# Optimization experiments

Measured on AMD Instinct MI355X. Metric: run time of the kernel, lower is better.

Reference implementation:

```python
import jax, jax.numpy as jnp
import numpy as np
from jax import lax

# Dims: B queries, N nodes, E edges (inverse edges already included), D hidden,
# R2 = 2*num_relation, T tail candidates, M text-embedded nodes, L layers.
B, N, E, D, R2, T, M, L = 4, 50000, 1600000, 64, 1000, 32, 10000, 3
NODE_RATIO, DEG_RATIO = 0.1, 1.0
K = int(NODE_RATIO * N)              # nodes kept per layer (variadic_topks on node scores)
ESEL = int(DEG_RATIO * K * E / N)    # edges kept per layer


def setup_inputs():
    key = jax.random.key(0)
    ks = jax.random.split(key, 16)
    f32 = jnp.float32
    return {
        "h_index": jax.random.randint(ks[0], (B,), 0, N),
        "r_index": jax.random.randint(ks[1], (B,), 0, R2),
        "t_index": jax.random.randint(ks[2], (B, T), 0, N),
        "all_index": jax.random.randint(ks[3], (M,), 0, N),
        "edge_src": jax.random.randint(ks[4], (E,), 0, N),
        "edge_dst": jax.random.randint(ks[5], (E,), 0, N),
        "edge_type": jax.random.randint(ks[6], (E,), 0, R2),
        "hidden_states": jax.random.normal(ks[7], (B, D), f32),
        "score_text_embs": jax.random.normal(ks[8], (M, D), f32),
        "rel_table": 0.02 * jax.random.normal(ks[9], (R2, D), f32),
        "linear_w": jax.random.normal(ks[10], (2 * D, D), f32) / np.sqrt(2 * D),
        "linear_b": jnp.zeros((D,), f32),
        "mlp_w1": jax.random.normal(ks[11], (D, 2 * D), f32) / np.sqrt(D),
        "mlp_b1": jnp.zeros((2 * D,), f32),
        "mlp_w2": jax.random.normal(ks[12], (2 * D, 1), f32) / np.sqrt(2 * D),
        "mlp_b2": jnp.zeros((1,), f32),
        "relw": 0.1 * jax.random.normal(ks[13], (L, R2, D), f32),
        "pna_w": jax.random.normal(ks[14], (L, 12 * D, D), f32) / np.sqrt(12 * D),
        "pna_b": jnp.zeros((L, D), f32),
    }


def _forward(h_index, r_index, t_index, all_index, edge_src, edge_dst, edge_type,
             hidden_states, score_text_embs, rel_table, linear_w, linear_b,
             mlp_w1, mlp_b1, mlp_w2, mlp_b2, relw, pna_w, pna_b):
    def score_fn(hidden, rel):  # hidden [n, D], rel [D] -> [n]
        rel_b = jnp.broadcast_to(rel, hidden.shape)
        heur = jnp.concatenate([hidden, rel_b], -1) @ linear_w + linear_b
        x = hidden * heur
        h1 = jax.nn.relu(x @ mlp_w1 + mlp_b1)
        return jnp.squeeze(h1 @ mlp_w2 + mlp_b2, -1)

    # pna_degree_mean = mean(log(degree_out + 1)) over the base graph
    deg_out_full = jax.ops.segment_sum(jnp.ones((E,), jnp.float32), edge_src, num_segments=N)
    dmean = jnp.mean(jnp.log(deg_out_full + 1.0))

    rel_embeds = rel_table[r_index]  # [B, D]

    def per_batch(rel, h_idx, head_emb, t_idx):
        # init_input_embeds: text embeddings at all_index, head embedding at h_idx
        hidden = (jnp.zeros((N, D), jnp.float32)
                  .at[all_index].set(score_text_embs)
                  .at[h_idx].set(head_emb))
        base = score_fn(jnp.zeros((1, D), jnp.float32), rel)[0]
        score = jnp.full((N,), base, jnp.float32).at[h_idx].set(score_fn(head_emb[None], rel)[0])

        for l in range(L):
            # ---- select_edges: top-K nodes by score, then top-ESEL outgoing edges by dst score
            _, nidx = lax.top_k(score, K)
            sel = jnp.zeros((N,), bool).at[nidx].set(True)
            escore = jnp.where(sel[edge_src], score[edge_dst], -jnp.inf)
            ev, eidx = lax.top_k(escore, ESEL)
            valid = jnp.isfinite(ev)
            s, d, et = edge_src[eidx], edge_dst[eidx], edge_type[eidx]

            # ---- gated message passing on the selected subgraph (PNA aggregation)
            gate = jax.nn.sigmoid(score)
            msg = (gate[s, None] * hidden[s]) * relw[l][et]        # [ESEL, D]
            msg0 = jnp.where(valid[:, None], msg, 0.0)
            deg = jax.ops.segment_sum(valid.astype(jnp.float32), d, num_segments=N)
            sm = jax.ops.segment_sum(msg0, d, num_segments=N)
            sq = jax.ops.segment_sum(msg0 * msg0, d, num_segments=N)
            mx = jax.ops.segment_max(jnp.where(valid[:, None], msg, -jnp.inf), d, num_segments=N)
            mn = jax.ops.segment_min(jnp.where(valid[:, None], msg, jnp.inf), d, num_segments=N)
            has = (deg > 0.0)[:, None]
            degc = jnp.maximum(deg, 1.0)[:, None]
            mean = sm / degc
            std = jnp.where(has, jnp.sqrt(jax.nn.relu(sq / degc - mean * mean) + 1e-6), 0.0)
            mx = jnp.where(has, mx, 0.0)
            mn = jnp.where(has, mn, 0.0)
            logd = jnp.log(deg + 1.0)[:, None]
            amp = logd / dmean
            att = jnp.where(has, dmean / jnp.maximum(logd, 1e-6), 0.0)
            one = jnp.ones_like(amp)
            # 4 aggregators x 3 degree scalers -> [N, 12D]
            feats = jnp.concatenate([a * sc for a in (mean, mx, mn, std) for sc in (one, amp, att)], -1)
            out = feats @ pna_w[l] + pna_b[l]

            # scatter back: only nodes with subgraph out-degree > 0 are updated
            hidden = jnp.where(has, hidden + out, hidden)
            score = jnp.where(deg > 0.0, score_fn(hidden, rel), score)
        return score[t_idx]

    return jax.vmap(per_batch)(rel_embeds, h_index, hidden_states, t_index)  # [B, T]


def reference(h_index, r_index, t_index, all_index, edge_src, edge_dst, edge_type,
              hidden_states, score_text_embs, rel_table, linear_w, linear_b,
              mlp_w1, mlp_b1, mlp_w2, mlp_b2, relw, pna_w, pna_b):
    return _forward(h_index, r_index, t_index, all_index, edge_src, edge_dst, edge_type,
                    hidden_states, score_text_embs, rel_table, linear_w, linear_b,
                    mlp_w1, mlp_b1, mlp_w2, mlp_b2, relw, pna_w, pna_b)
```

## Files before the change

kernel.cpp:

```cpp
#include <hip/hip_runtime.h>
#include <cstdint>
#include <cstddef>


#define NN   50000
#define NEG  1600000
#define NR2  1000
#define NTC  32
#define NMI  10000
#define KSEL 5000u
#define ESEL 160000u
#define KEY_NEG_INF 0x007FFFFFu

#define OFF_ST    0
#define OFF_RELB  64
#define OFF_BC    128
#define OFF_BC2   2176
#define OFF_HISTA 4224
#define OFF_HISTB 69760
#define OFF_SCORE 135296
#define OFF_NSEL  185296
#define OFF_DCNT  235296
#define OFF_ROWS  285296
#define OFF_CURS  335296
#define OFF_ACT   385296
#define OFF_HID   435296
#define OFF_SRCH  3635296
#define OFF_ELIST 3955296
#define OFF_CSR   4115296
#define OFF_BALG  (OFF_CSR + 50032)
#define SBLK      4275296

#define RL(x,k) __int_as_float(__builtin_amdgcn_readlane(__float_as_int(x),(k)))
#define BBASE unsigned* B = WB + (size_t)blockIdx.y * (size_t)sb

__device__ inline unsigned fkey(float f){
  unsigned u = __float_as_uint(f);
  if ((u << 1) == 0u) u = 0u;
  return (u & 0x80000000u) ? ~u : (u | 0x80000000u);
}

__device__ inline float waveSumF(float v){
  #pragma unroll
  for (int d = 1; d < 64; d <<= 1) v += __shfl_xor(v, d);
  return v;
}

__device__ inline void ldsHashAdd(unsigned* hkey, unsigned* hval, unsigned bin, unsigned cnt){
  unsigned h = (bin * 2654435761u) >> 23;
  while (true){
    unsigned prev = atomicCAS(hkey + h, 0xFFFFFFFFu, bin);
    if (prev == 0xFFFFFFFFu || prev == bin){ atomicAdd(hval + h, cnt); return; }
    h = (h + 1u) & 511u;
  }
}


__global__ void k_lastm(const int* __restrict__ all_index, int* __restrict__ lastm){
  int i = blockIdx.x * 256 + threadIdx.x;
  if (i < NMI) atomicMax(lastm + all_index[i], i);
}

__global__ void k_degfull(const int* __restrict__ esrc, unsigned* __restrict__ degf){
  int i = blockIdx.x * 256 + threadIdx.x;
  if (i < NEG) atomicAdd(degf + esrc[i], 1u);
}

__global__ void k_dsum(const unsigned* __restrict__ degf, float* __restrict__ gstF){
  int i = blockIdx.x * 256 + threadIdx.x;
  float v = (i < NN) ? logf((float)degf[i] + 1.f) : 0.f;
  v = waveSumF(v);
  if ((threadIdx.x & 63) == 0) atomicAdd(gstF + 4, v);
}

__global__ void k_finalize(float* __restrict__ gstF, const float* __restrict__ b1,
                           const float* __restrict__ w2, const float* __restrict__ b2){
  gstF[5] = gstF[4] / (float)NN;
  float s = 0.f;
  for (int m = 0; m < 128; m++) s += fmaxf(b1[m], 0.f) * w2[m];
  gstF[6] = s + b2[0];
}


__global__ void k_relb(unsigned* WB, long sb, int b0,
                       const int* __restrict__ r_index, const float* __restrict__ hs,
                       const float* __restrict__ rel_table, const float* __restrict__ lw,
                       const float* __restrict__ lb, const float* __restrict__ w1,
                       const float* __restrict__ b1, const float* __restrict__ w2,
                       const float* __restrict__ b2){
  BBASE;
  float* relb = (float*)(B + OFF_RELB);
  float* stF  = (float*)(B + OFF_ST);
  int b = b0 + blockIdx.y;
  int j = threadIdx.x;
  int r = r_index[b];
  float acc = lb[j];
  for (int k = 0; k < 64; k++) acc = fmaf(rel_table[(size_t)r*64 + k], lw[(64 + k)*64 + j], acc);
  relb[j] = acc;
  float heur = acc;
  for (int k = 0; k < 64; k++) heur = fmaf(hs[b*64 + k], lw[k*64 + j], heur);
  float x = hs[b*64 + j] * heur;
  float o = 0.f;
  for (int half = 0; half < 2; half++){
    float a = b1[half*64 + j];
    for (int k = 0; k < 64; k++) a = fmaf(__shfl(x, k), w1[k*128 + half*64 + j], a);
    o = fmaf(fmaxf(a, 0.f), w2[half*64 + j], o);
  }
  o = waveSumF(o);
  if (j == 0) stF[7] = o + b2[0];
}

__global__ void k_inithidden(unsigned* WB, long sb, int b0,
                             const int* __restrict__ lastm, const float* __restrict__ ste,
                             const float* __restrict__ hs, const int* __restrict__ h_index){
  BBASE;
  float4* hidden = (float4*)(B + OFF_HID);
  const float4* ste4 = (const float4*)ste;
  const float4* hs4  = (const float4*)hs;
  int b = b0 + blockIdx.y;
  int idx = blockIdx.x * 256 + threadIdx.x;
  int n = idx >> 4, j = idx & 15;
  int h = h_index[b];
  float4 v = make_float4(0.f, 0.f, 0.f, 0.f);
  int lm = lastm[n];
  if (lm >= 0) v = ste4[(size_t)lm*16 + j];
  if (n == h)  v = hs4[b*16 + j];
  hidden[idx] = v;
}

__global__ void k_initscore(unsigned* WB, long sb, int b0,
                            const int* __restrict__ h_index, const float* __restrict__ gstF){
  BBASE;
  float* score = (float*)(B + OFF_SCORE);
  unsigned* st = B + OFF_ST;
  float* stF = (float*)st;
  int b = b0 + blockIdx.y;
  int i = blockIdx.x * 256 + threadIdx.x;
  if (i < NN) score[i] = (i == h_index[b]) ? stF[7] : gstF[6];
  if (i == 0){ st[0] = 0u; st[1] = KSEL; }
}


__global__ __launch_bounds__(256) void k_hist(unsigned* WB, long sb, int pass){
  BBASE;
  const unsigned* st = B + OFF_ST;
  const float* score = (const float*)(B + OFF_SCORE);
  unsigned* hist = B + ((pass == 1) ? OFF_HISTA : OFF_HISTB);
  __shared__ unsigned hkey[512];
  __shared__ unsigned hval[512];
  for (int t = threadIdx.x; t < 512; t += 256){ hkey[t] = 0xFFFFFFFFu; hval[t] = 0u; }
  __syncthreads();
  int i = blockIdx.x * 256 + threadIdx.x;
  unsigned bin = 0xFFFFFFFFu;
  if (i < NN){
    unsigned k = fkey(score[i]);
    if (pass == 1) bin = k >> 16;
    else if ((k >> 16) == (st[0] >> 16)) bin = k & 0xFFFFu;
  }
  bool active = (bin != 0xFFFFFFFFu);
  int lane = threadIdx.x & 63;
  #pragma unroll
  for (int r = 0; r < 2; r++){
    unsigned long long mask = __ballot((int)active);
    if (mask != 0ull){
      int leader = __ffsll(mask) - 1;
      unsigned lbin = (unsigned)__shfl((int)bin, leader);
      bool same = active && (bin == lbin);
      unsigned long long smask = __ballot((int)same);
      if (lane == leader) ldsHashAdd(hkey, hval, lbin, (unsigned)__popcll(smask));
      if (same) active = false;
    }
  }
  if (active) ldsHashAdd(hkey, hval, bin, 1u);
  __syncthreads();
  for (int t = threadIdx.x; t < 512; t += 256){
    unsigned vv = hval[t];
    if (vv) atomicAdd(hist + hkey[t], vv);
  }
}

__global__ void k_indegW(unsigned* WB, long sb,
                         const int* __restrict__ esrc, const int* __restrict__ edst){
  BBASE;
  unsigned* st = B + OFF_ST;
  const unsigned* nsel = B + OFF_NSEL;
  unsigned* indeg = B + OFF_CURS;
  int i = blockIdx.x * 256 + threadIdx.x;
  if (i < NEG && nsel[esrc[i]]) atomicAdd(indeg + edst[i], 1u);
  if (i == 0){ st[0] = 0u; st[1] = ESEL; st[2] = 0u; st[3] = 0u; st[4] = 0u; st[5] = 0u; }
}

__global__ __launch_bounds__(256) void k_histW(unsigned* WB, long sb, int pass){
  BBASE;
  const unsigned* st = B + OFF_ST;
  const unsigned* indeg = B + OFF_CURS;
  const float* score = (const float*)(B + OFF_SCORE);
  unsigned* hist = B + ((pass == 1) ? OFF_HISTA : OFF_HISTB);
  __shared__ unsigned hkey[512];
  __shared__ unsigned hval[512];
  for (int t = threadIdx.x; t < 512; t += 256){ hkey[t] = 0xFFFFFFFFu; hval[t] = 0u; }
  __syncthreads();
  int i = blockIdx.x * 256 + threadIdx.x;
  unsigned w = (i < NN) ? indeg[i] : 0u;
  if (w){
    unsigned k = fkey(score[i]);
    unsigned bin = 0xFFFFFFFFu;
    if (pass == 1) bin = k >> 16;
    else if ((k >> 16) == (st[0] >> 16)) bin = k & 0xFFFFu;
    if (bin != 0xFFFFFFFFu) ldsHashAdd(hkey, hval, bin, w);
  }
  __syncthreads();
  for (int t = threadIdx.x; t < 512; t += 256){
    unsigned vv = hval[t];
    if (vv) atomicAdd(hist + hkey[t], vv);
  }
}

__global__ __launch_bounds__(1024) void k_pick16(unsigned* WB, long sb, int pass){
  BBASE;
  unsigned* st = B + OFF_ST;
  const unsigned* hist = B + ((pass == 1) ? OFF_HISTA : OFF_HISTB);
  __shared__ unsigned csum[1024];
  __shared__ unsigned sc[1024];
  int t = threadIdx.x;
  unsigned R = st[1];
  unsigned s = 0;
  {
    const unsigned* hp = hist + (unsigned)t * 64u;
    for (int b = 0; b < 64; b++) s += hp[b];
  }
  csum[t] = s; sc[t] = s; __syncthreads();
  for (int d = 1; d < 1024; d <<= 1){
    unsigned v = (t >= d) ? sc[t - d] : 0u;
    __syncthreads();
    sc[t] += v;
    __syncthreads();
  }
  unsigned total = sc[1023];
  unsigned above = total - sc[t];
  unsigned cs = csum[t];
  if (above < R && above + cs >= R){
    unsigned cum = above;
    for (int b = 63; b >= 0; b--){
      unsigned c = hist[(unsigned)(t*64 + b)];
      if (cum + c >= R){
        unsigned bstar = (unsigned)(t*64 + b);
        if (pass == 1) st[0] = bstar << 16; else st[0] = st[0] | bstar;
        st[1] = R - cum;
        break;
      }
      cum += c;
    }
  }
  if (t == 0 && total < R){
    if (pass == 1) st[0] = KEY_NEG_INF & 0xFFFF0000u;
    else           st[0] = st[0] | 0xFFFFu;
    st[1] = R - total;
  }
}

__global__ __launch_bounds__(1024) void k_countEq(unsigned* WB, long sb, int mode, int n,
                                                  const int* __restrict__ esrc,
                                                  const int* __restrict__ edst){
  BBASE;
  unsigned* hz = B + OFF_HISTA;
  for (unsigned j = blockIdx.x * 1024u + threadIdx.x; j < 131072u; j += gridDim.x * 1024u)
    hz[j] = 0u;
  unsigned* dcnt = B + OFF_DCNT;
  const unsigned* st = B + OFF_ST;
  const unsigned* nsel = B + OFF_NSEL;
  const float* score = (const float*)(B + OFF_SCORE);
  unsigned* bcE = B + OFF_BC;
  unsigned* bcG = B + OFF_BC2;
  unsigned* balE = B + OFF_CSR;
  unsigned* balG = B + OFF_BALG;
  int i = blockIdx.x * 1024 + threadIdx.x;
  if (i < NN) dcnt[i] = 0u;
  unsigned v = st[0];
  unsigned k = 0u;
  if (i < n){
    if (mode) k = nsel[esrc[i]] ? fkey(score[edst[i]]) : KEY_NEG_INF;
    else      k = fkey(score[i]);
  }
  bool eq = (i < n) && (k == v);
  bool gt = (i < n) && (k > v);
  unsigned long long ebal = __ballot((int)eq);
  unsigned long long gbal = __ballot((int)gt);
  __shared__ unsigned wshE[16];
  __shared__ unsigned wshG[16];
  int wid = threadIdx.x >> 6, lane = threadIdx.x & 63;
  if (mode && lane == 0){
    int gw = blockIdx.x * 16 + wid;
    balE[2*gw]     = (unsigned)ebal;
    balE[2*gw + 1] = (unsigned)(ebal >> 32);
    balG[2*gw]     = (unsigned)gbal;
    balG[2*gw + 1] = (unsigned)(gbal >> 32);
  }
  if (lane == 0){ wshE[wid] = (unsigned)__popcll(ebal); wshG[wid] = (unsigned)__popcll(gbal); }
  __syncthreads();
  if (threadIdx.x == 0){
    unsigned te = 0, tg = 0;
    for (int w = 0; w < 16; w++){ te += wshE[w]; tg += wshG[w]; }
    bcE[blockIdx.x] = te; bcG[blockIdx.x] = tg;
  }
}

__global__ __launch_bounds__(1024) void k_scanBlocks(unsigned* WB, long sb, int nbk){
  BBASE;
  unsigned* blockcnt = B + OFF_BC;
  __shared__ unsigned sc[2048];
  int t = threadIdx.x;
  unsigned a  = (t < nbk) ? blockcnt[t] : 0u;
  unsigned b2 = (1024 + t < nbk) ? blockcnt[1024 + t] : 0u;
  sc[t] = a; sc[1024 + t] = b2; __syncthreads();
  for (int d = 1; d < 2048; d <<= 1){
    unsigned v1 = (t >= d) ? sc[t - d] : 0u;
    unsigned v2 = (1024 + t >= d) ? sc[1024 + t - d] : 0u;
    __syncthreads();
    sc[t] += v1; sc[1024 + t] += v2;
    __syncthreads();
  }
  if (t < nbk) blockcnt[t] = sc[t] - a;
  if (1024 + t < nbk) blockcnt[1024 + t] = sc[1024 + t] - b2;
}

__global__ __launch_bounds__(1024) void k_scanBlocks2(unsigned* WB, long sb, int nbk){
  BBASE;
  unsigned* st = B + OFF_ST;
  unsigned* bcE = B + OFF_BC;
  unsigned* bcG = B + OFF_BC2;
  __shared__ unsigned se[2048];
  __shared__ unsigned sg[2048];
  int t = threadIdx.x;
  unsigned e0 = (t < nbk) ? bcE[t] : 0u;
  unsigned e1 = (1024 + t < nbk) ? bcE[1024 + t] : 0u;
  unsigned g0 = (t < nbk) ? bcG[t] : 0u;
  unsigned g1 = (1024 + t < nbk) ? bcG[1024 + t] : 0u;
  se[t] = e0; se[1024 + t] = e1; sg[t] = g0; sg[1024 + t] = g1;
  __syncthreads();
  for (int d = 1; d < 2048; d <<= 1){
    unsigned a1 = (t >= d) ? se[t - d] : 0u;
    unsigned a2 = (1024 + t >= d) ? se[1024 + t - d] : 0u;
    unsigned c1 = (t >= d) ? sg[t - d] : 0u;
    unsigned c2 = (1024 + t >= d) ? sg[1024 + t - d] : 0u;
    __syncthreads();
    se[t] += a1; se[1024 + t] += a2; sg[t] += c1; sg[1024 + t] += c2;
    __syncthreads();
  }
  if (t < nbk) bcE[t] = se[t] - e0;
  if (1024 + t < nbk) bcE[1024 + t] = se[1024 + t] - e1;
  if (t < nbk) bcG[t] = sg[t] - g0;
  if (1024 + t < nbk) bcG[1024 + t] = sg[1024 + t] - g1;
  if (t == 0){
    unsigned gtTot = sg[2047];
    st[4] = gtTot;
    st[2] = gtTot + ((st[0] > KEY_NEG_INF) ? st[1] : 0u);
  }
}

__global__ __launch_bounds__(1024) void k_selNodes(unsigned* WB, long sb){
  BBASE;
  const unsigned* st = B + OFF_ST;
  const unsigned* blockcnt = B + OFF_BC;
  const float* score = (const float*)(B + OFF_SCORE);
  unsigned* nsel = B + OFF_NSEL;
  unsigned* curs = B + OFF_CURS;
  int i = blockIdx.x * 1024 + threadIdx.x;
  if (i < NN) curs[i] = 0u;
  unsigned v = st[0], R = st[1];
  unsigned k = (i < NN) ? fkey(score[i]) : 0u;
  bool eq = (i < NN) && (k == v);
  unsigned long long bal = __ballot((int)eq);
  __shared__ unsigned wsh[16];
  int wid = threadIdx.x >> 6, lane = threadIdx.x & 63;
  if (lane == 0) wsh[wid] = (unsigned)__popcll(bal);
  __syncthreads();
  unsigned woff = 0;
  for (int w = 0; w < wid; w++) woff += wsh[w];
  unsigned lpre = (unsigned)__popcll(bal & ((1ull << lane) - 1ull));
  unsigned rank = blockcnt[blockIdx.x] + woff + lpre;
  if (i < NN) nsel[i] = (k > v || (eq && rank < R)) ? 1u : 0u;
}

__global__ __launch_bounds__(1024) void k_selEdgesCompact(unsigned* WB, long sb,
                                                          const int* __restrict__ esrc,
                                                          const int* __restrict__ edst){
  BBASE;
  const unsigned* st = B + OFF_ST;
  const unsigned* bcE = B + OFF_BC;
  const unsigned* bcG = B + OFF_BC2;
  const unsigned* balE = B + OFF_CSR;
  const unsigned* balG = B + OFF_BALG;
  unsigned* elist = B + OFF_ELIST;
  unsigned* dcnt = B + OFF_DCNT;
  int i = blockIdx.x * 1024 + threadIdx.x;
  unsigned v = st[0], R = st[1], gtTot = st[4];
  int wid = threadIdx.x >> 6, lane = threadIdx.x & 63;
  int gw = blockIdx.x * 16 + wid;
  unsigned long long ebal = ((unsigned long long)balE[2*gw + 1] << 32) | balE[2*gw];
  unsigned long long gbal = ((unsigned long long)balG[2*gw + 1] << 32) | balG[2*gw];
  bool eq = (ebal >> lane) & 1ull;
  bool gt = (gbal >> lane) & 1ull;
  __shared__ unsigned wshE[16];
  __shared__ unsigned wshG[16];
  if (lane == 0){ wshE[wid] = (unsigned)__popcll(ebal); wshG[wid] = (unsigned)__popcll(gbal); }
  __syncthreads();
  unsigned eoff = 0, goff = 0;
  for (int w = 0; w < 16 && w < wid; w++){ eoff += wshE[w]; goff += wshG[w]; }
  unsigned long long ltm = (1ull << lane) - 1ull;
  if (gt){
    elist[bcG[blockIdx.x] + goff + (unsigned)__popcll(gbal & ltm)] = (unsigned)i;
    atomicAdd(dcnt + edst[i], 1u);
  }
  if (eq){
    unsigned rank = bcE[blockIdx.x] + eoff + (unsigned)__popcll(ebal & ltm);
    if (v > KEY_NEG_INF && rank < R){
      elist[gtTot + rank] = (unsigned)i;
      atomicAdd(dcnt + edst[i], 1u);
    }
  }
}


__global__ __launch_bounds__(1024) void k_blocksumsInt(unsigned* WB, long sb){
  BBASE;
  const unsigned* dcnt = B + OFF_DCNT;
  unsigned* blockcnt = B + OFF_BC;
  int i = blockIdx.x * 1024 + threadIdx.x;
  unsigned v = (i < NN) ? dcnt[i] : 0u;
  #pragma unroll
  for (int d = 1; d < 64; d <<= 1) v += (unsigned)__shfl_xor((int)v, d);
  __shared__ unsigned wsh[16];
  int wid = threadIdx.x >> 6, lane = threadIdx.x & 63;
  if (lane == 0) wsh[wid] = v;
  __syncthreads();
  if (threadIdx.x == 0){
    unsigned tot = 0;
    for (int w = 0; w < 16; w++) tot += wsh[w];
    blockcnt[blockIdx.x] = tot;
  }
}

__global__ __launch_bounds__(1024) void k_rowSnap(unsigned* WB, long sb){
  BBASE;
  unsigned* st = B + OFF_ST;
  const unsigned* dcnt = B + OFF_DCNT;
  const unsigned* blockcnt = B + OFF_BC;
  unsigned* rowstart = B + OFF_ROWS;
  unsigned* curs = B + OFF_CURS;
  unsigned* actl = B + OFF_ACT;
  unsigned* srcmap = B + OFF_NSEL;
  const float* score = (const float*)(B + OFF_SCORE);
  const float* hidden = (const float*)(B + OFF_HID);
  float* srch = (float*)(B + OFF_SRCH);
  int i = blockIdx.x * 1024 + threadIdx.x;
  int wid = threadIdx.x >> 6, lane = threadIdx.x & 63;
  unsigned d = (i < NN) ? dcnt[i] : 0u;
  unsigned v = d;
  #pragma unroll
  for (int dl = 1; dl < 64; dl <<= 1){
    unsigned t2 = (unsigned)__shfl_up((int)v, dl);
    if (lane >= dl) v += t2;
  }
  bool act = (i < NN) && (d > 0u);
  unsigned long long abal = __ballot((int)act);
  __shared__ unsigned wsh[16];
  __shared__ unsigned awsh[16];
  __shared__ unsigned abase;
  if (lane == 63) wsh[wid] = v;
  if (lane == 0) awsh[wid] = (unsigned)__popcll(abal);
  __syncthreads();
  if (threadIdx.x == 0){
    unsigned tot = 0;
    for (int w = 0; w < 16; w++) tot += awsh[w];
    abase = atomicAdd(st + 3, tot);
  }
  unsigned woff = 0, aoff = 0;
  for (int w = 0; w < wid; w++){ woff += wsh[w]; aoff += awsh[w]; }
  __syncthreads();
  unsigned excl = blockcnt[blockIdx.x] + woff + (v - d);
  if (i < NN){ rowstart[i] = excl; curs[i] = excl; }
  if (act) actl[abase + aoff + (unsigned)__popcll(abal & ((1ull << lane) - 1ull))] = (unsigned)i;

  int base = i - lane;
  if (base >= NN) return;
  bool sel = (i < NN) && (srcmap[i] != 0u);
  unsigned long long bal = __ballot((int)sel);
  if (bal == 0ull) return;
  unsigned slotbase = 0;
  if (lane == 0) slotbase = atomicAdd(st + 5, (unsigned)__popcll(bal));
  slotbase = (unsigned)__shfl((int)slotbase, 0);
  unsigned long long m2 = bal;
  unsigned idx = 0;
  while (m2){
    int j = __ffsll(m2) - 1;
    m2 = m2 - (m2 bitand (0ull - m2));
    int node = base + j;
    unsigned slot = slotbase + idx; idx++;
    if (lane == 0) srcmap[node] = slot;
    float g = 1.f / (1.f + expf(-score[node]));
    srch[(size_t)slot*64 + lane] = g * hidden[(size_t)node*64 + lane];
  }
}

__global__ void k_scatter(unsigned* WB, long sb, const int* __restrict__ esrc,
                          const int* __restrict__ edst, const int* __restrict__ etype){
  BBASE;
  const unsigned* st = B + OFF_ST;
  const unsigned* elist = B + OFF_ELIST;
  const unsigned* srcmap = B + OFF_NSEL;
  unsigned* curs = B + OFF_CURS;
  unsigned* csr = B + OFF_CSR;
  unsigned i = blockIdx.x * 256 + threadIdx.x;
  if (i < st[2]){
    unsigned e = elist[i];
    unsigned slot = srcmap[esrc[e]];
    unsigned pk = (slot << 10) | (unsigned)etype[e];
    unsigned pos = atomicAdd(curs + edst[e], 1u);
    csr[pos] = pk;
  }
}


__global__ __launch_bounds__(256) void k_aggpna(unsigned* WB, long sb,
    const float* __restrict__ relw, const float* __restrict__ pw,
    const float* __restrict__ pb, const float* __restrict__ gstF, int l){
  BBASE;
  const unsigned* st = B + OFF_ST;
  const unsigned* actl = B + OFF_ACT;
  const unsigned* dcnt = B + OFF_DCNT;
  const unsigned* rows = B + OFF_ROWS;
  const unsigned* csr = B + OFF_CSR;
  const float* srch = (const float*)(B + OFF_SRCH);
  float* hidden = (float*)(B + OFF_HID);
  const float* relw_l = relw + (size_t)l * NR2 * 64;
  const float* pw_l = pw + (size_t)l * 768 * 64;

  __shared__ float aggL[64 * 64];

  int lane = threadIdx.x & 63;
  int w = threadIdx.x >> 6;
  unsigned nact = st[3];
  unsigned nbase = (unsigned)blockIdx.x * 64u;
  if (nbase >= nact) return;
  float dmean = gstF[5];

  unsigned slotM = nbase + (unsigned)lane;
  int nodeM = (slotM < nact) ? (int)actl[slotM] : -1;
  float dvM = (nodeM >= 0) ? (float)dcnt[nodeM] : 0.f;
  float logd = logf(dvM + 1.f);
  float ampv = logd / dmean;
  float attv = dmean / fmaxf(logd, 1e-6f);
  int jbase = __builtin_amdgcn_readfirstlane((int)(threadIdx.x >> 6)) * 16;
  float acc[16];
  #pragma unroll
  for (int jj = 0; jj < 16; jj++) acc[jj] = pb[(size_t)l*64 + jbase + jj];

  int nodeG[16]; unsigned cntG[16], rsG[16];
  #pragma unroll
  for (int i = 0; i < 16; i++){
    unsigned slot = nbase + (unsigned)(w * 16 + i);
    nodeG[i] = (slot < nact) ? (int)actl[slot] : -1;
  }
  #pragma unroll
  for (int i = 0; i < 16; i++){
    cntG[i] = (nodeG[i] >= 0) ? dcnt[nodeG[i]] : 0u;
    rsG[i]  = (nodeG[i] >= 0) ? rows[nodeG[i]] : 0u;
  }

  float mxS[16], mnS[16], sdS[16];
  #pragma unroll
  for (int g = 0; g < 4; g++){
    unsigned pkA[4], pkB[4], pkC[4], pkD[4];
    #pragma unroll
    for (int q = 0; q < 4; q++){
      int i = g*4 + q;
      unsigned cnt = cntG[i], rs = rsG[i];
      bool vld = (nodeG[i] >= 0);
      unsigned c1 = (1u < cnt) ? 1u : 0u;
      unsigned c2 = (2u < cnt) ? 2u : 0u;
      unsigned c3 = (3u < cnt) ? 3u : 0u;
      pkA[q] = vld ? csr[rs]      : 0u;
      pkB[q] = vld ? csr[rs + c1] : 0u;
      pkC[q] = vld ? csr[rs + c2] : 0u;
      pkD[q] = vld ? csr[rs + c3] : 0u;
    }
    #pragma unroll
    for (int q = 0; q < 4; q++){
      int i = g*4 + q;
      int nloc = w * 16 + i;
      float pmean = 0.f;
      mxS[i] = 0.f; mnS[i] = 0.f; sdS[i] = 0.f;
      if (nodeG[i] >= 0){
        unsigned cnt = cntG[i], rs = rsG[i];
        float sm_ = 0.f, sq_ = 0.f;
        float mx_ = -__builtin_huge_valf(), mn_ = __builtin_huge_valf();
        {
          unsigned pk0 = pkA[q], pk1 = pkB[q], pk2 = pkC[q], pk3 = pkD[q];
          float s0 = srch[(size_t)(pk0 >> 10)*64 + lane];
          float r0 = relw_l[(size_t)(pk0 & 1023u)*64 + lane];
          float s1 = srch[(size_t)(pk1 >> 10)*64 + lane];
          float r1 = relw_l[(size_t)(pk1 & 1023u)*64 + lane];
          float s2 = srch[(size_t)(pk2 >> 10)*64 + lane];
          float r2 = relw_l[(size_t)(pk2 & 1023u)*64 + lane];
          float s3 = srch[(size_t)(pk3 >> 10)*64 + lane];
          float r3 = relw_l[(size_t)(pk3 & 1023u)*64 + lane];
          float m = s0 * r0;
          sm_ += m; sq_ = fmaf(m, m, sq_); mx_ = fmaxf(mx_, m); mn_ = fminf(mn_, m);
          if (1u < cnt){
            m = s1 * r1;
            sm_ += m; sq_ = fmaf(m, m, sq_); mx_ = fmaxf(mx_, m); mn_ = fminf(mn_, m);
          }
          if (2u < cnt){
            m = s2 * r2;
            sm_ += m; sq_ = fmaf(m, m, sq_); mx_ = fmaxf(mx_, m); mn_ = fminf(mn_, m);
          }
          if (3u < cnt){
            m = s3 * r3;
            sm_ += m; sq_ = fmaf(m, m, sq_); mx_ = fmaxf(mx_, m); mn_ = fminf(mn_, m);
          }
        }
        for (unsigned ii = 4; ii < cnt; ii += 4u){
          unsigned i1 = (ii + 1u < cnt) ? ii + 1u : ii;
          unsigned i2 = (ii + 2u < cnt) ? ii + 2u : ii;
          unsigned i3 = (ii + 3u < cnt) ? ii + 3u : ii;
          unsigned pk0 = csr[rs + ii];
          unsigned pk1 = csr[rs + i1];
          unsigned pk2 = csr[rs + i2];
          unsigned pk3 = csr[rs + i3];
          float s0 = srch[(size_t)(pk0 >> 10)*64 + lane];
          float r0 = relw_l[(size_t)(pk0 & 1023u)*64 + lane];
          float s1 = srch[(size_t)(pk1 >> 10)*64 + lane];
          float r1 = relw_l[(size_t)(pk1 & 1023u)*64 + lane];
          float s2 = srch[(size_t)(pk2 >> 10)*64 + lane];
          float r2 = relw_l[(size_t)(pk2 & 1023u)*64 + lane];
          float s3 = srch[(size_t)(pk3 >> 10)*64 + lane];
          float r3 = relw_l[(size_t)(pk3 & 1023u)*64 + lane];
          float m = s0 * r0;
          sm_ += m; sq_ = fmaf(m, m, sq_); mx_ = fmaxf(mx_, m); mn_ = fminf(mn_, m);
          if (ii + 1u < cnt){
            m = s1 * r1;
            sm_ += m; sq_ = fmaf(m, m, sq_); mx_ = fmaxf(mx_, m); mn_ = fminf(mn_, m);
          }
          if (ii + 2u < cnt){
            m = s2 * r2;
            sm_ += m; sq_ = fmaf(m, m, sq_); mx_ = fmaxf(mx_, m); mn_ = fminf(mn_, m);
          }
          if (ii + 3u < cnt){
            m = s3 * r3;
            sm_ += m; sq_ = fmaf(m, m, sq_); mx_ = fmaxf(mx_, m); mn_ = fminf(mn_, m);
          }
        }
        float dv = (float)cnt;
        float degc = fmaxf(dv, 1.f);
        float me = sm_ / degc;
        pmean = me;
        mxS[i] = mx_;
        mnS[i] = mn_;
        sdS[i] = sqrtf(fmaxf(sq_ / degc - me*me, 0.f) + 1e-6f);
      }
      aggL[lane*64 + (nloc ^ lane)] = pmean;
    }
  }

  for (int p = 0; p < 4; p++){
    if (p){
      __syncthreads();
      #pragma unroll
      for (int i = 0; i < 16; i++){
        int nloc = w * 16 + i;
        float v = (p == 1) ? mxS[i] : ((p == 2) ? mnS[i] : sdS[i]);
        aggL[lane*64 + (nloc ^ lane)] = v;
      }
    }
    __syncthreads();
    for (int cc = 0; cc < 3; cc++){
      int c = p*3 + cc;
      float sc = (cc == 0) ? 1.f : ((cc == 1) ? ampv : attv);
      const float* wc = pw_l + (size_t)c*64*64 + jbase;
      #pragma unroll 4
      for (int k = 0; k < 64; k++){
        float fv = aggL[k*64 + (lane ^ k)] * sc;
        const float* wp = wc + (size_t)k*64;
        #pragma unroll
        for (int jj = 0; jj < 16; jj++)
          acc[jj] = fmaf(fv, wp[jj], acc[jj]);
      }
    }
  }
  if (nodeM >= 0){
    float* hp = hidden + (size_t)nodeM*64 + jbase;
    #pragma unroll
    for (int q = 0; q < 4; q++){
      float4 h = *(float4*)(hp + q*4);
      h.x += acc[q*4+0]; h.y += acc[q*4+1]; h.z += acc[q*4+2]; h.w += acc[q*4+3];
      *(float4*)(hp + q*4) = h;
    }
  }
}


__global__ __launch_bounds__(256) void k_scoreK(unsigned* WB, long sb,
    const float* __restrict__ lw, const float* __restrict__ w1,
    const float* __restrict__ b1, const float* __restrict__ w2,
    const float* __restrict__ b2){
  BBASE;
  unsigned* st = B + OFF_ST;
  if (blockIdx.x == 0 && threadIdx.x == 0){ st[0] = 0u; st[1] = KSEL; }
  const unsigned* actl = B + OFF_ACT;
  const float* hidden = (const float*)(B + OFF_HID);
  const float* relb = (const float*)(B + OFF_RELB);
  float* score = (float*)(B + OFF_SCORE);

  __shared__ float P0[64 * 64];
  __shared__ float P1[64 * 64];

  int lane = threadIdx.x & 63;
  int w = threadIdx.x >> 6;
  unsigned nact = st[3];
  unsigned nbase = (unsigned)blockIdx.x * 64u;
  if (nbase >= nact) return;

  int nodeG[16];
  #pragma unroll
  for (int i = 0; i < 16; i++){
    unsigned slot = nbase + (unsigned)(w * 16 + i);
    nodeG[i] = (slot < nact) ? (int)actl[slot] : -1;
  }
  #pragma unroll
  for (int i = 0; i < 16; i++){
    int nloc = w * 16 + i;
    float hv = (nodeG[i] >= 0) ? hidden[(size_t)nodeG[i]*64 + lane] : 0.f;
    P0[lane*64 + (nloc ^ lane)] = hv;
  }
  __syncthreads();

  int jb = __builtin_amdgcn_readfirstlane(w) * 16;
  float heur[16];
  #pragma unroll
  for (int i = 0; i < 16; i++) heur[i] = relb[jb + i];
  #pragma unroll 4
  for (int k = 0; k < 64; k++){
    float hk = P0[k*64 + (lane ^ k)];
    const float* lwk = lw + k*64 + jb;
    #pragma unroll
    for (int i = 0; i < 16; i++) heur[i] = fmaf(hk, lwk[i], heur[i]);
  }
  #pragma unroll
  for (int i = 0; i < 16; i++){
    int j = jb + i;
    float hj = P0[j*64 + (lane ^ j)];
    P1[j*64 + (lane ^ j)] = hj * heur[i];
  }
  __syncthreads();

  float alo[16], ahi[16];
  #pragma unroll
  for (int mm = 0; mm < 16; mm++){ alo[mm] = b1[jb + mm]; ahi[mm] = b1[64 + jb + mm]; }
  #pragma unroll 4
  for (int j = 0; j < 64; j++){
    float xj = P1[j*64 + (lane ^ j)];
    const float* w1j = w1 + j*128;
    #pragma unroll
    for (int mm = 0; mm < 16; mm++){
      alo[mm] = fmaf(xj, w1j[jb + mm], alo[mm]);
      ahi[mm] = fmaf(xj, w1j[64 + jb + mm], ahi[mm]);
    }
  }
  #pragma unroll
  for (int mm = 0; mm < 16; mm++){
    int j = jb + mm;
    float p = fmaf(fmaxf(alo[mm], 0.f), w2[j], 0.f);
    p = fmaf(fmaxf(ahi[mm], 0.f), w2[64 + j], p);
    P0[j*64 + (lane ^ j)] = p;
  }
  __syncthreads();

  float b2v = b2[0];
  for (int i = 0; i < 16; i++){
    int nloc = w * 16 + i;
    unsigned slot = nbase + (unsigned)nloc;
    float p = P0[lane*64 + (nloc ^ lane)];
    float r = waveSumF(p);
    if (lane == 0 && slot < nact) score[(int)actl[slot]] = r + b2v;
  }
}

__global__ void k_out(unsigned* WB, long sb, int b0,
                      const int* __restrict__ t_index, float* __restrict__ out){
  BBASE;
  const float* score = (const float*)(B + OFF_SCORE);
  int b = b0 + blockIdx.y;
  int t = threadIdx.x;
  if (t < NTC) out[b*NTC + t] = score[t_index[b*NTC + t]];
}


extern "C" void kernel_launch(void* const* d_in, const int* in_sizes, int n_in,
                              void* d_out, int out_size, void* d_ws, size_t ws_size,
                              hipStream_t stream){
  (void)in_sizes; (void)n_in; (void)out_size;
  const int*   h_index  = (const int*)d_in[0];
  const int*   r_index  = (const int*)d_in[1];
  const int*   t_index  = (const int*)d_in[2];
  const int*   all_idx  = (const int*)d_in[3];
  const int*   esrc     = (const int*)d_in[4];
  const int*   edst     = (const int*)d_in[5];
  const int*   etype    = (const int*)d_in[6];
  const float* hs       = (const float*)d_in[7];
  const float* ste      = (const float*)d_in[8];
  const float* rel_tab  = (const float*)d_in[9];
  const float* lw       = (const float*)d_in[10];
  const float* lb       = (const float*)d_in[11];
  const float* w1       = (const float*)d_in[12];
  const float* b1       = (const float*)d_in[13];
  const float* w2       = (const float*)d_in[14];
  const float* b2       = (const float*)d_in[15];
  const float* relw     = (const float*)d_in[16];
  const float* pna_w    = (const float*)d_in[17];
  const float* pna_b    = (const float*)d_in[18];
  float* out = (float*)d_out;

  unsigned* W = (unsigned*)d_ws;
  int*      LASTM = (int*)W;
  unsigned* DEGF  = W + 50000;
  float*    GSTF  = (float*)(W + 100000);
  unsigned* WB    = W + 100064;

  size_t needB = (size_t)(100064 + 4*(size_t)SBLK) * 4u;
  int nb; long sb; int nseq;
  if (ws_size >= needB){ nb = 4; sb = SBLK; nseq = 1; }
  else                 { nb = 1; sb = 0;    nseq = 4; }

  (void)hipMemsetAsync(W + 100000, 0, 64 * 4, stream);
  (void)hipMemsetAsync(LASTM, 0xFF, NN * 4, stream);
  (void)hipMemsetAsync(DEGF, 0, NN * 4, stream);
  for (int q = 0; q < nb; q++)
    (void)hipMemsetAsync(WB + (size_t)q*SBLK + OFF_HISTA, 0, 131072 * 4, stream);

  const int GB_E256  = (NEG + 255) / 256;
  const int GB_N256  = (NN + 255) / 256;
  const int GB_N1024 = (NN + 1023) / 1024;
  const int GB_E1024 = (NEG + 1023) / 1024;
  const int GB_H4    = (NN * 16) / 256;
  const int GB_A2    = (NN + 63) / 64;
  const int GB_ES    = (int)(ESEL / 256);

  k_lastm<<<(NMI + 255) / 256, 256, 0, stream>>>(all_idx, LASTM);
  k_degfull<<<GB_E256, 256, 0, stream>>>(esrc, DEGF);
  k_dsum<<<GB_N256, 256, 0, stream>>>(DEGF, GSTF);
  k_finalize<<<1, 1, 0, stream>>>(GSTF, b1, w2, b2);

  for (int q = 0; q < nseq; q++){
    int b0 = (nb == 4) ? 0 : q;
    k_relb<<<dim3(1, nb), 64, 0, stream>>>(WB, sb, b0, r_index, hs, rel_tab, lw, lb, w1, b1, w2, b2);
    k_inithidden<<<dim3(GB_H4, nb), 256, 0, stream>>>(WB, sb, b0, LASTM, ste, hs, h_index);
    k_initscore<<<dim3(GB_N256, nb), 256, 0, stream>>>(WB, sb, b0, h_index, GSTF);

    for (int l = 0; l < 3; l++){
      k_hist<<<dim3(GB_N256, nb), 256, 0, stream>>>(WB, sb, 1);
      k_pick16<<<dim3(1, nb), 1024, 0, stream>>>(WB, sb, 1);
      k_hist<<<dim3(GB_N256, nb), 256, 0, stream>>>(WB, sb, 0);
      k_pick16<<<dim3(1, nb), 1024, 0, stream>>>(WB, sb, 0);
      k_countEq<<<dim3(GB_N1024, nb), 1024, 0, stream>>>(WB, sb, 0, NN, esrc, edst);
      k_scanBlocks<<<dim3(1, nb), 1024, 0, stream>>>(WB, sb, GB_N1024);
      k_selNodes<<<dim3(GB_N1024, nb), 1024, 0, stream>>>(WB, sb);
      k_indegW<<<dim3(GB_E256, nb), 256, 0, stream>>>(WB, sb, esrc, edst);
      k_histW<<<dim3(GB_N256, nb), 256, 0, stream>>>(WB, sb, 1);
      k_pick16<<<dim3(1, nb), 1024, 0, stream>>>(WB, sb, 1);
      k_histW<<<dim3(GB_N256, nb), 256, 0, stream>>>(WB, sb, 0);
      k_pick16<<<dim3(1, nb), 1024, 0, stream>>>(WB, sb, 0);
      k_countEq<<<dim3(GB_E1024, nb), 1024, 0, stream>>>(WB, sb, 1, NEG, esrc, edst);
      k_scanBlocks2<<<dim3(1, nb), 1024, 0, stream>>>(WB, sb, GB_E1024);
      k_selEdgesCompact<<<dim3(GB_E1024, nb), 1024, 0, stream>>>(WB, sb, esrc, edst);
      k_blocksumsInt<<<dim3(GB_N1024, nb), 1024, 0, stream>>>(WB, sb);
      k_scanBlocks<<<dim3(1, nb), 1024, 0, stream>>>(WB, sb, GB_N1024);
      k_rowSnap<<<dim3(GB_N1024, nb), 1024, 0, stream>>>(WB, sb);
      k_scatter<<<dim3(GB_ES, nb), 256, 0, stream>>>(WB, sb, esrc, edst, etype);
      k_aggpna<<<dim3(GB_A2, nb), 256, 0, stream>>>(WB, sb, relw, pna_w, pna_b, GSTF, l);
      k_scoreK<<<dim3(GB_A2, nb), 256, 0, stream>>>(WB, sb, lw, w1, b1, w2, b2);
    }
    k_out<<<dim3(1, nb), 32, 0, stream>>>(WB, sb, b0, t_index, out);
  }
}
```

Measured before the change: 2.233 ms.

## Drop separate block-scan kernels and cache edge selection ballots from indegree pass

Removes the three single-block scan kernels per layer. Each consumer block now computes its own exclusive prefix by summing the preceding block counts directly: a serial loop for the node kernels, and a wave-shuffle reduction over up to 1563 counts for the edge compaction kernel. The indegree kernel also stores per-wave ballots of whether each edge's source is selected, so the edge counting pass reads a bit instead of gathering nsel[esrc[i]]. This cuts kernel launches and dependent gathers, but adds redundant prefix work in every block.

```diff
diff --git a/kernel.cpp b/kernel.cpp
--- a/kernel.cpp
+++ b/kernel.cpp
@@ -11,6 +11,8 @@
 #define KSEL 5000u
 #define ESEL 160000u
 #define KEY_NEG_INF 0x007FFFFFu
+#define NEBK 1563
+#define NWAVE_E (NEG/64)
 
 #define OFF_ST    0
 #define OFF_RELB  64
@@ -185,8 +187,17 @@
   unsigned* st = B + OFF_ST;
   const unsigned* nsel = B + OFF_NSEL;
   unsigned* indeg = B + OFF_CURS;
+  unsigned* sbal = B + OFF_ELIST;
   int i = blockIdx.x * 256 + threadIdx.x;
-  if (i < NEG && nsel[esrc[i]]) atomicAdd(indeg + edst[i], 1u);
+  int wid = threadIdx.x >> 6, lane = threadIdx.x & 63;
+  bool s = nsel[esrc[i]] != 0u;
+  unsigned long long bal = __ballot((int)s);
+  if (s) atomicAdd(indeg + edst[i], 1u);
+  if (lane == 0){
+    int gw = blockIdx.x * 4 + wid;
+    sbal[2*gw]     = (unsigned)bal;
+    sbal[2*gw + 1] = (unsigned)(bal >> 32);
+  }
   if (i == 0){ st[0] = 0u; st[1] = ESEL; st[2] = 0u; st[3] = 0u; st[4] = 0u; st[5] = 0u; }
 }
 
@@ -268,7 +279,6 @@
     hz[j] = 0u;
   unsigned* dcnt = B + OFF_DCNT;
   const unsigned* st = B + OFF_ST;
-  const unsigned* nsel = B + OFF_NSEL;
   const float* score = (const float*)(B + OFF_SCORE);
   unsigned* bcE = B + OFF_BC;
   unsigned* bcG = B + OFF_BC2;
@@ -277,18 +287,29 @@
   int i = blockIdx.x * 1024 + threadIdx.x;
   if (i < NN) dcnt[i] = 0u;
   unsigned v = st[0];
-  unsigned k = 0u;
-  if (i < n){
-    if (mode) k = nsel[esrc[i]] ? fkey(score[edst[i]]) : KEY_NEG_INF;
-    else      k = fkey(score[i]);
-  }
-  bool eq = (i < n) && (k == v);
-  bool gt = (i < n) && (k > v);
+  int wid = threadIdx.x >> 6, lane = threadIdx.x & 63;
+  bool eq = false, gt = false;
+  if (mode){
+    const unsigned* sbal = B + OFF_ELIST;
+    int gw = blockIdx.x * 16 + wid;
+    if (gw < NWAVE_E){
+      unsigned long long sb64 = ((unsigned long long)sbal[2*gw + 1] << 32) | sbal[2*gw];
+      bool ssel = (sb64 >> lane) & 1ull;
+      unsigned k = KEY_NEG_INF;
+      if (ssel) k = fkey(score[edst[i]]);
+      eq = (k == v);
+      gt = (k > v);
+    }
+  } else {
+    unsigned k = 0u;
+    if (i < n) k = fkey(score[i]);
+    eq = (i < n) && (k == v);
+    gt = (i < n) && (k > v);
+  }
   unsigned long long ebal = __ballot((int)eq);
   unsigned long long gbal = __ballot((int)gt);
   __shared__ unsigned wshE[16];
   __shared__ unsigned wshG[16];
-  int wid = threadIdx.x >> 6, lane = threadIdx.x & 63;
   if (mode && lane == 0){
     int gw = blockIdx.x * 16 + wid;
     balE[2*gw]     = (unsigned)ebal;
@@ -302,59 +323,6 @@
     unsigned te = 0, tg = 0;
     for (int w = 0; w < 16; w++){ te += wshE[w]; tg += wshG[w]; }
     bcE[blockIdx.x] = te; bcG[blockIdx.x] = tg;
-  }
-}
-
-__global__ __launch_bounds__(1024) void k_scanBlocks(unsigned* WB, long sb, int nbk){
-  BBASE;
-  unsigned* blockcnt = B + OFF_BC;
-  __shared__ unsigned sc[2048];
-  int t = threadIdx.x;
-  unsigned a  = (t < nbk) ? blockcnt[t] : 0u;
-  unsigned b2 = (1024 + t < nbk) ? blockcnt[1024 + t] : 0u;
-  sc[t] = a; sc[1024 + t] = b2; __syncthreads();
-  for (int d = 1; d < 2048; d <<= 1){
-    unsigned v1 = (t >= d) ? sc[t - d] : 0u;
-    unsigned v2 = (1024 + t >= d) ? sc[1024 + t - d] : 0u;
-    __syncthreads();
-    sc[t] += v1; sc[1024 + t] += v2;
-    __syncthreads();
-  }
-  if (t < nbk) blockcnt[t] = sc[t] - a;
-  if (1024 + t < nbk) blockcnt[1024 + t] = sc[1024 + t] - b2;
-}
-
-__global__ __launch_bounds__(1024) void k_scanBlocks2(unsigned* WB, long sb, int nbk){
-  BBASE;
-  unsigned* st = B + OFF_ST;
-  unsigned* bcE = B + OFF_BC;
-  unsigned* bcG = B + OFF_BC2;
-  __shared__ unsigned se[2048];
-  __shared__ unsigned sg[2048];
-  int t = threadIdx.x;
-  unsigned e0 = (t < nbk) ? bcE[t] : 0u;
-  unsigned e1 = (1024 + t < nbk) ? bcE[1024 + t] : 0u;
-  unsigned g0 = (t < nbk) ? bcG[t] : 0u;
-  unsigned g1 = (1024 + t < nbk) ? bcG[1024 + t] : 0u;
-  se[t] = e0; se[1024 + t] = e1; sg[t] = g0; sg[1024 + t] = g1;
-  __syncthreads();
-  for (int d = 1; d < 2048; d <<= 1){
-    unsigned a1 = (t >= d) ? se[t - d] : 0u;
-    unsigned a2 = (1024 + t >= d) ? se[1024 + t - d] : 0u;
-    unsigned c1 = (t >= d) ? sg[t - d] : 0u;
-    unsigned c2 = (1024 + t >= d) ? sg[1024 + t - d] : 0u;
-    __syncthreads();
-    se[t] += a1; se[1024 + t] += a2; sg[t] += c1; sg[1024 + t] += c2;
-    __syncthreads();
-  }
-  if (t < nbk) bcE[t] = se[t] - e0;
-  if (1024 + t < nbk) bcE[1024 + t] = se[1024 + t] - e1;
-  if (t < nbk) bcG[t] = sg[t] - g0;
-  if (1024 + t < nbk) bcG[1024 + t] = sg[1024 + t] - g1;
-  if (t == 0){
-    unsigned gtTot = sg[2047];
-    st[4] = gtTot;
-    st[2] = gtTot + ((st[0] > KEY_NEG_INF) ? st[1] : 0u);
   }
 }
 
@@ -375,10 +343,12 @@
   int wid = threadIdx.x >> 6, lane = threadIdx.x & 63;
   if (lane == 0) wsh[wid] = (unsigned)__popcll(bal);
   __syncthreads();
+  unsigned pre = 0;
+  for (int bn = 0; bn < blockIdx.x; bn++) pre += blockcnt[bn];
   unsigned woff = 0;
   for (int w = 0; w < wid; w++) woff += wsh[w];
   unsigned lpre = (unsigned)__popcll(bal & ((1ull << lane) - 1ull));
-  unsigned rank = blockcnt[blockIdx.x] + woff + lpre;
+  unsigned rank = pre + woff + lpre;
   if (i < NN) nsel[i] = (k > v || (eq && rank < R)) ? 1u : 0u;
 }
 
@@ -386,7 +356,7 @@
                                                           const int* __restrict__ esrc,
                                                           const int* __restrict__ edst){
   BBASE;
-  const unsigned* st = B + OFF_ST;
+  unsigned* st = B + OFF_ST;
   const unsigned* bcE = B + OFF_BC;
   const unsigned* bcG = B + OFF_BC2;
   const unsigned* balE = B + OFF_CSR;
@@ -394,26 +364,46 @@
   unsigned* elist = B + OFF_ELIST;
   unsigned* dcnt = B + OFF_DCNT;
   int i = blockIdx.x * 1024 + threadIdx.x;
-  unsigned v = st[0], R = st[1], gtTot = st[4];
+  unsigned v = st[0], R = st[1];
+  int t = threadIdx.x;
   int wid = threadIdx.x >> 6, lane = threadIdx.x & 63;
   int gw = blockIdx.x * 16 + wid;
   unsigned long long ebal = ((unsigned long long)balE[2*gw + 1] << 32) | balE[2*gw];
   unsigned long long gbal = ((unsigned long long)balG[2*gw + 1] << 32) | balG[2*gw];
   bool eq = (ebal >> lane) & 1ull;
   bool gt = (gbal >> lane) & 1ull;
-  __shared__ unsigned wshE[16];
-  __shared__ unsigned wshG[16];
-  if (lane == 0){ wshE[wid] = (unsigned)__popcll(ebal); wshG[wid] = (unsigned)__popcll(gbal); }
-  __syncthreads();
+  unsigned eP = 0, gP = 0, gT = 0;
+  if (t < blockIdx.x){ eP = bcE[t]; gP = bcG[t]; }
+  if (1024 + t < blockIdx.x){ eP += bcE[1024 + t]; gP += bcG[1024 + t]; }
+  if (t < NEBK) gT = bcG[t];
+  if (1024 + t < NEBK) gT += bcG[1024 + t];
+  #pragma unroll
+  for (int d = 1; d < 64; d <<= 1){
+    eP += (unsigned)__shfl_xor((int)eP, d);
+    gP += (unsigned)__shfl_xor((int)gP, d);
+    gT += (unsigned)__shfl_xor((int)gT, d);
+  }
+  __shared__ unsigned wE[16], wG[16], wT[16], wshE[16], wshG[16];
+  if (lane == 0){
+    wE[wid] = eP; wG[wid] = gP; wT[wid] = gT;
+    wshE[wid] = (unsigned)__popcll(ebal); wshG[wid] = (unsigned)__popcll(gbal);
+  }
+  __syncthreads();
+  unsigned eBase = 0, gBase = 0, gtTot = 0;
+  for (int w = 0; w < 16; w++){ eBase += wE[w]; gBase += wG[w]; gtTot += wT[w]; }
   unsigned eoff = 0, goff = 0;
-  for (int w = 0; w < 16 && w < wid; w++){ eoff += wshE[w]; goff += wshG[w]; }
+  for (int w = 0; w < wid; w++){ eoff += wshE[w]; goff += wshG[w]; }
+  if (blockIdx.x == 0 && threadIdx.x == 0){
+    st[4] = gtTot;
+    st[2] = gtTot + ((v > KEY_NEG_INF) ? R : 0u);
+  }
   unsigned long long ltm = (1ull << lane) - 1ull;
   if (gt){
-    elist[bcG[blockIdx.x] + goff + (unsigned)__popcll(gbal & ltm)] = (unsigned)i;
+    elist[gBase + goff + (unsigned)__popcll(gbal & ltm)] = (unsigned)i;
     atomicAdd(dcnt + edst[i], 1u);
   }
   if (eq){
-    unsigned rank = bcE[blockIdx.x] + eoff + (unsigned)__popcll(ebal & ltm);
+    unsigned rank = eBase + eoff + (unsigned)__popcll(ebal & ltm);
     if (v > KEY_NEG_INF && rank < R){
       elist[gtTot + rank] = (unsigned)i;
       atomicAdd(dcnt + edst[i], 1u);
@@ -475,10 +465,12 @@
     for (int w = 0; w < 16; w++) tot += awsh[w];
     abase = atomicAdd(st + 3, tot);
   }
+  unsigned pre = 0;
+  for (int bn = 0; bn < blockIdx.x; bn++) pre += blockcnt[bn];
   unsigned woff = 0, aoff = 0;
   for (int w = 0; w < wid; w++){ woff += wsh[w]; aoff += awsh[w]; }
   __syncthreads();
-  unsigned excl = blockcnt[blockIdx.x] + woff + (v - d);
+  unsigned excl = pre + woff + (v - d);
   if (i < NN){ rowstart[i] = excl; curs[i] = excl; }
   if (act) actl[abase + aoff + (unsigned)__popcll(abal & ((1ull << lane) - 1ull))] = (unsigned)i;
 
@@ -863,7 +855,6 @@
       k_hist<<<dim3(GB_N256, nb), 256, 0, stream>>>(WB, sb, 0);
       k_pick16<<<dim3(1, nb), 1024, 0, stream>>>(WB, sb, 0);
       k_countEq<<<dim3(GB_N1024, nb), 1024, 0, stream>>>(WB, sb, 0, NN, esrc, edst);
-      k_scanBlocks<<<dim3(1, nb), 1024, 0, stream>>>(WB, sb, GB_N1024);
       k_selNodes<<<dim3(GB_N1024, nb), 1024, 0, stream>>>(WB, sb);
       k_indegW<<<dim3(GB_E256, nb), 256, 0, stream>>>(WB, sb, esrc, edst);
       k_histW<<<dim3(GB_N256, nb), 256, 0, stream>>>(WB, sb, 1);
@@ -871,10 +862,8 @@
       k_histW<<<dim3(GB_N256, nb), 256, 0, stream>>>(WB, sb, 0);
       k_pick16<<<dim3(1, nb), 1024, 0, stream>>>(WB, sb, 0);
       k_countEq<<<dim3(GB_E1024, nb), 1024, 0, stream>>>(WB, sb, 1, NEG, esrc, edst);
-      k_scanBlocks2<<<dim3(1, nb), 1024, 0, stream>>>(WB, sb, GB_E1024);
       k_selEdgesCompact<<<dim3(GB_E1024, nb), 1024, 0, stream>>>(WB, sb, esrc, edst);
       k_blocksumsInt<<<dim3(GB_N1024, nb), 1024, 0, stream>>>(WB, sb);
-      k_scanBlocks<<<dim3(1, nb), 1024, 0, stream>>>(WB, sb, GB_N1024);
       k_rowSnap<<<dim3(GB_N1024, nb), 1024, 0, stream>>>(WB, sb);
       k_scatter<<<dim3(GB_ES, nb), 256, 0, stream>>>(WB, sb, esrc, edst, etype);
       k_aggpna<<<dim3(GB_A2, nb), 256, 0, stream>>>(WB, sb, relw, pna_w, pna_b, GSTF, l);
```

Result: slower. 2.280 ms (+2.1%).
